# Optimization experiments

Measured on AMD Instinct MI355X. Metric: run time of the kernel, lower is better.

## Reference

```python
import jax, jax.numpy as jnp
import numpy as np
import math

N_NODES = 100000
N_EDGES = 1600000
IN_DIM = 32
OUT_DIM = 32

def setup_inputs() -> dict:
    key = jax.random.key(0)
    k1, k2, k3, k4 = jax.random.split(key, 4)
    X = jax.random.normal(k1, (N_NODES, IN_DIM), dtype=jnp.float32)
    src_idx = jax.random.randint(k2, (N_EDGES,), 0, N_NODES, dtype=jnp.int64)
    dst_idx = jax.random.randint(k3, (N_EDGES,), 0, N_NODES, dtype=jnp.int64)
    # weights init: uniform(-stdv, stdv), stdv = 1/sqrt(output_dim)
    stdv = 1.0 / math.sqrt(OUT_DIM)
    W = jax.random.uniform(k4, (IN_DIM, OUT_DIM), dtype=jnp.float32,
                           minval=-stdv, maxval=stdv)
    return {"X": X, "W": W, "src_idx": src_idx, "dst_idx": dst_idx}

def reference(X, W, src_idx, dst_idx):
    # GIN sum-aggregation SpMM: agg[i] = sum_{j in N(i)} X[j]
    agg = jax.ops.segment_sum(X[src_idx], dst_idx, num_segments=N_NODES)
    # dense GEMM: X_prime = agg @ W
    return agg @ W
```

## Files before the change

kernel.cpp:

```cpp
#include <hip/hip_runtime.h>

#define N_DIM 32
#define NPB 64
#define NB_FINE_MAX 2048
#define NC_MAX 128
#define CSH 10
#define CAPC 18432
#define CAPFINE 1280
#define CEPB 4096
#define FT 512
#define GROWS 512
#define CAPF 2048
#define MAXCH 10

__device__ __forceinline__ unsigned f2bf_rne(float f) {
    unsigned u = __float_as_uint(f);
    return (u + 0x7FFFu + ((u >> 16) & 1u)) >> 16;
}
__device__ __forceinline__ float bf2f(unsigned h) {
    return __uint_as_float(h << 16);
}

__global__ __launch_bounds__(FT) void k_fused(const float* __restrict__ X,
                                              const float* __restrict__ W,
                                              unsigned* __restrict__ Y,
                                              const int* __restrict__ src,
                                              const int* __restrict__ dst,
                                              int* __restrict__ cursorC0,
                                              int* __restrict__ tmp,
                                              int n_nodes, int n_edges,
                                              int ncoarse, int nblk_g) {
    __shared__ float Wlds[N_DIM * N_DIM];
    __shared__ int h[NC_MAX];
    __shared__ int gb[NC_MAX];
    const int t = threadIdx.x;

    if (blockIdx.x < nblk_g) {
        for (int i = t; i < N_DIM * N_DIM; i += FT) Wlds[i] = W[i];
        __syncthreads();
        const int r = blockIdx.x * GROWS + t;
        if (r >= n_nodes) return;

        float x[N_DIM];
        const float4* xr = (const float4*)(X + (size_t)r * N_DIM);
#pragma unroll
        for (int i = 0; i < N_DIM / 4; ++i) {
            float4 v = xr[i];
            x[4 * i + 0] = v.x; x[4 * i + 1] = v.y;
            x[4 * i + 2] = v.z; x[4 * i + 3] = v.w;
        }
        float acc[N_DIM];
#pragma unroll
        for (int c = 0; c < N_DIM; ++c) acc[c] = 0.0f;
#pragma unroll
        for (int k = 0; k < N_DIM; ++k) {
            const float xk = x[k];
#pragma unroll
            for (int c = 0; c < N_DIM; ++c)
                acc[c] = fmaf(xk, Wlds[k * N_DIM + c], acc[c]);
        }
        unsigned yp[16];
#pragma unroll
        for (int q = 0; q < 16; ++q)
            yp[q] = f2bf_rne(acc[2 * q]) | (f2bf_rne(acc[2 * q + 1]) << 16);
        uint4* yr = (uint4*)(Y + (size_t)r * 16);
#pragma unroll
        for (int i = 0; i < 4; ++i)
            yr[i] = make_uint4(yp[4 * i], yp[4 * i + 1],
                               yp[4 * i + 2], yp[4 * i + 3]);
    } else {
        if (t < NC_MAX) h[t] = 0;
        __syncthreads();
        const int start = (blockIdx.x - nblk_g) * CEPB;

        int vw[CEPB / FT], cw[CEPB / FT], rw[CEPB / FT];
#pragma unroll
        for (int k = 0; k < CEPB / FT; ++k) {
            int e = start + t + k * FT;
            if (e < n_edges) {
                int d = dst[e];
                int c = d >> CSH;
                cw[k] = c;
                vw[k] = src[e] | ((d & 1023) << 17);
                rw[k] = atomicAdd(&h[c], 1);
            } else {
                cw[k] = -1;
            }
        }
        __syncthreads();
        if (t < ncoarse) {
            int c = h[t];
            gb[t] = c ? atomicAdd(&cursorC0[t], c) : 0;
        }
        __syncthreads();
#pragma unroll
        for (int k = 0; k < CEPB / FT; ++k)
            if (cw[k] >= 0) {
                int idx = gb[cw[k]] + rw[k];
                if (idx < CAPC) tmp[cw[k] * CAPC + idx] = vw[k];
            }
    }
}

__global__ __launch_bounds__(256) void k_fpart(const int* __restrict__ tmp,
                                               const int* __restrict__ cursorC0,
                                               int* __restrict__ cursorF0,
                                               int* __restrict__ pairs,
                                               int ncoarse) {
    __shared__ int cnt[16], gpos[16];
    const int t = threadIdx.x;
    const int c = blockIdx.x;
    const int lenC = min(cursorC0[c], CAPC);

    for (int chunk = blockIdx.y; chunk * CAPF < lenC; chunk += gridDim.y) {
        const int start = chunk * CAPF;
        const int n = min(CAPF, lenC - start);
        if (t < 16) cnt[t] = 0;
        __syncthreads();
        int pv[CAPF / 256], rv[CAPF / 256];
#pragma unroll
        for (int k = 0; k < CAPF / 256; ++k) {
            int i = t + k * 256;
            if (i < n) {
                int p = tmp[c * CAPC + start + i];
                pv[k] = p;
                rv[k] = atomicAdd(&cnt[(p >> 23) & 15], 1);
            } else {
                pv[k] = -1;
            }
        }
        __syncthreads();
        if (t < 16) gpos[t] = cnt[t] ? atomicAdd(&cursorF0[16 * c + t], cnt[t]) : 0;
        __syncthreads();
#pragma unroll
        for (int k = 0; k < CAPF / 256; ++k) {
            if (pv[k] >= 0) {
                int p = pv[k];
                int f = (p >> 23) & 15;
                int idx = gpos[f] + rv[k];
                if (idx < CAPFINE)
                    pairs[(size_t)(16 * c + f) * CAPFINE + idx] = p & 0x7FFFFF;
            }
        }
        __syncthreads();
    }
}

__device__ __forceinline__ void addv(float* acc, uint4 v) {
    acc[0] += bf2f(v.x & 0xFFFFu); acc[1] += bf2f(v.x >> 16);
    acc[2] += bf2f(v.y & 0xFFFFu); acc[3] += bf2f(v.y >> 16);
    acc[4] += bf2f(v.z & 0xFFFFu); acc[5] += bf2f(v.z >> 16);
    acc[6] += bf2f(v.w & 0xFFFFu); acc[7] += bf2f(v.w >> 16);
}

__global__ __launch_bounds__(256) void k_agg(const uint4* __restrict__ Y4,
                                             const int* __restrict__ cursorF0,
                                             const int* __restrict__ pairs,
                                             float* __restrict__ out,
                                             int n_nodes) {
    __shared__ int sbin[CAPFINE];
    __shared__ int cnt[NPB];
    __shared__ int cst[NPB];
    __shared__ int excl[NPB];

    const int t = threadIdx.x;
    const int b = blockIdx.x;
    const int len = min(cursorF0[b], CAPFINE);
    const size_t segbase = (size_t)b * CAPFINE;
    const int g = t >> 2;
    const int l = t & 3;

    if (t < NPB) cnt[t] = 0;
    __syncthreads();

    int pv[CAPFINE / 256], rv[CAPFINE / 256];
#pragma unroll
    for (int k = 0; k < CAPFINE / 256; ++k) {
        int i = t + k * 256;
        if (i < len) {
            int p = pairs[segbase + i];
            pv[k] = p;
            rv[k] = atomicAdd(&cnt[p >> 17], 1);
        } else {
            pv[k] = -1;
        }
    }
    __syncthreads();
    if (t < 64) {
        int c0 = cnt[t];
        int c = c0;
#pragma unroll
        for (int off = 1; off < 64; off <<= 1) {
            int u = __shfl_up(c, off, 64);
            if (t >= off) c += u;
        }
        cst[t] = c;
        excl[t] = c - c0;
    }
    __syncthreads();
#pragma unroll
    for (int k = 0; k < CAPFINE / 256; ++k) {
        if (pv[k] >= 0) {
            int p = pv[k];
            sbin[excl[p >> 17] + rv[k]] = p & 0x1FFFF;
        }
    }
    __syncthreads();

    float acc[8];
#pragma unroll
    for (int i = 0; i < 8; ++i) acc[i] = 0.0f;

    const int s1 = cst[g];
    const int s0 = s1 - cnt[g];
    for (int e = s0; e < s1; e += 4) {
        const int m = s1 - e;
        int i0 = sbin[e];
        int i1 = sbin[e + ((m > 1) ? 1 : 0)];
        int i2 = sbin[e + ((m > 2) ? 2 : 0)];
        int i3 = sbin[e + ((m > 3) ? 3 : 0)];
        uint4 v0 = Y4[(size_t)i0 * 4 + l];
        uint4 v1 = Y4[(size_t)i1 * 4 + l];
        uint4 v2 = Y4[(size_t)i2 * 4 + l];
        uint4 v3 = Y4[(size_t)i3 * 4 + l];
        addv(acc, v0);
        if (m > 1) addv(acc, v1);
        if (m > 2) addv(acc, v2);
        if (m > 3) addv(acc, v3);
    }

    const int node = b * NPB + g;
    if (node < n_nodes) {
        ((float4*)out)[(size_t)node * 8 + 2 * l] =
            make_float4(acc[0], acc[1], acc[2], acc[3]);
        ((float4*)out)[(size_t)node * 8 + 2 * l + 1] =
            make_float4(acc[4], acc[5], acc[6], acc[7]);
    }
}

extern "C" void kernel_launch(void* const* d_in, const int* in_sizes, int n_in,
                              void* d_out, int out_size, void* d_ws, size_t ws_size,
                              hipStream_t stream) {
    const float* X   = (const float*)d_in[0];
    const float* W   = (const float*)d_in[1];
    const int*   src = (const int*)d_in[2];
    const int*   dst = (const int*)d_in[3];
    float* out = (float*)d_out;

    const int n_nodes = in_sizes[0] / N_DIM;
    const int n_edges = in_sizes[2];
    const int nb = (n_nodes + NPB - 1) / NPB;
    const int ncoarse = (n_nodes + 1023) / 1024;

    unsigned* Y   = (unsigned*)d_ws;
    int* cursorC0 = (int*)(Y + (size_t)n_nodes * 16);
    int* cursorF0 = cursorC0 + NC_MAX;
    int* tmp      = cursorF0 + NB_FINE_MAX;
    int* pairs    = tmp + (size_t)ncoarse * CAPC;

    const int nblk_g = (n_nodes + GROWS - 1) / GROWS;
    const int nblk_c = (n_edges + CEPB - 1) / CEPB;

    hipMemsetAsync(cursorC0, 0, (size_t)(NC_MAX + NB_FINE_MAX) * sizeof(int), stream);

    k_fused<<<nblk_g + nblk_c, FT, 0, stream>>>(X, W, Y, src, dst, cursorC0, tmp,
                                                n_nodes, n_edges, ncoarse, nblk_g);
    k_fpart<<<dim3(ncoarse, MAXCH), 256, 0, stream>>>(tmp, cursorC0, cursorF0,
                                                      pairs, ncoarse);
    k_agg<<<nb, 256, 0, stream>>>((const uint4*)Y, cursorF0, pairs, out, n_nodes);
}
```

Baseline: 127.3 us.

## Balance aggregation work by splitting sorted edges evenly across thread groups

The aggregation kernel no longer gives each 4-thread group one destination node. It now splits the block's sorted edge list into equal contiguous chunks per group. Each group accumulates runs of the same node in registers and flushes partial sums into a padded shared-memory accumulator with atomic adds, and the block then writes that accumulator to global memory. This targets load imbalance from uneven node degrees, at the cost of shared-memory atomics, extra LDS use and one more barrier.

```diff
diff --git a/kernel.cpp b/kernel.cpp
--- a/kernel.cpp
+++ b/kernel.cpp
@@ -12,6 +12,7 @@
 #define GROWS 512
 #define CAPF 2048
 #define MAXCH 10
+#define ACCW 36
 
 __device__ __forceinline__ unsigned f2bf_rne(float f) {
     unsigned u = __float_as_uint(f);
@@ -153,6 +154,16 @@
     acc[6] += bf2f(v.w & 0xFFFFu); acc[7] += bf2f(v.w >> 16);
 }
 
+__device__ __forceinline__ void flush8(float* __restrict__ accS, int node, int l,
+                                       float* __restrict__ a) {
+    float* ap = accS + node * ACCW + l * 8;
+#pragma unroll
+    for (int j = 0; j < 8; ++j) {
+        atomicAdd(ap + j, a[j]);
+        a[j] = 0.0f;
+    }
+}
+
 __global__ __launch_bounds__(256) void k_agg(const uint4* __restrict__ Y4,
                                              const int* __restrict__ cursorF0,
                                              const int* __restrict__ pairs,
@@ -160,17 +171,17 @@
                                              int n_nodes) {
     __shared__ int sbin[CAPFINE];
     __shared__ int cnt[NPB];
-    __shared__ int cst[NPB];
     __shared__ int excl[NPB];
+    __shared__ float accS[NPB * ACCW];
 
     const int t = threadIdx.x;
     const int b = blockIdx.x;
     const int len = min(cursorF0[b], CAPFINE);
     const size_t segbase = (size_t)b * CAPFINE;
-    const int g = t >> 2;
     const int l = t & 3;
 
     if (t < NPB) cnt[t] = 0;
+    for (int i = t; i < NPB * ACCW; i += 256) accS[i] = 0.0f;
     __syncthreads();
 
     int pv[CAPFINE / 256], rv[CAPFINE / 256];
@@ -194,7 +205,6 @@
             int u = __shfl_up(c, off, 64);
             if (t >= off) c += u;
         }
-        cst[t] = c;
         excl[t] = c - c0;
     }
     __syncthreads();
@@ -202,39 +212,65 @@
     for (int k = 0; k < CAPFINE / 256; ++k) {
         if (pv[k] >= 0) {
             int p = pv[k];
-            sbin[excl[p >> 17] + rv[k]] = p & 0x1FFFF;
-        }
-    }
-    __syncthreads();
-
-    float acc[8];
-#pragma unroll
-    for (int i = 0; i < 8; ++i) acc[i] = 0.0f;
-
-    const int s1 = cst[g];
-    const int s0 = s1 - cnt[g];
-    for (int e = s0; e < s1; e += 4) {
-        const int m = s1 - e;
-        int i0 = sbin[e];
-        int i1 = sbin[e + ((m > 1) ? 1 : 0)];
-        int i2 = sbin[e + ((m > 2) ? 2 : 0)];
-        int i3 = sbin[e + ((m > 3) ? 3 : 0)];
-        uint4 v0 = Y4[(size_t)i0 * 4 + l];
-        uint4 v1 = Y4[(size_t)i1 * 4 + l];
-        uint4 v2 = Y4[(size_t)i2 * 4 + l];
-        uint4 v3 = Y4[(size_t)i3 * 4 + l];
-        addv(acc, v0);
-        if (m > 1) addv(acc, v1);
-        if (m > 2) addv(acc, v2);
-        if (m > 3) addv(acc, v3);
-    }
-
-    const int node = b * NPB + g;
-    if (node < n_nodes) {
-        ((float4*)out)[(size_t)node * 8 + 2 * l] =
-            make_float4(acc[0], acc[1], acc[2], acc[3]);
-        ((float4*)out)[(size_t)node * 8 + 2 * l + 1] =
-            make_float4(acc[4], acc[5], acc[6], acc[7]);
+            sbin[excl[p >> 17] + rv[k]] = p;
+        }
+    }
+    __syncthreads();
+
+    const int s = t >> 2;
+    const int clen = (len + NPB - 1) >> 6;
+    const int e0 = s * clen;
+    const int e1 = min(e0 + clen, len);
+
+    float a[8];
+#pragma unroll
+    for (int i = 0; i < 8; ++i) a[i] = 0.0f;
+    int cur = -1;
+
+    for (int e = e0; e < e1; e += 4) {
+        const int m = e1 - e;
+        int p0 = sbin[e];
+        int p1 = sbin[e + ((m > 1) ? 1 : 0)];
+        int p2 = sbin[e + ((m > 2) ? 2 : 0)];
+        int p3 = sbin[e + ((m > 3) ? 3 : 0)];
+        uint4 v0 = Y4[(size_t)(p0 & 0x1FFFF) * 4 + l];
+        uint4 v1 = Y4[(size_t)(p1 & 0x1FFFF) * 4 + l];
+        uint4 v2 = Y4[(size_t)(p2 & 0x1FFFF) * 4 + l];
+        uint4 v3 = Y4[(size_t)(p3 & 0x1FFFF) * 4 + l];
+        int n0 = p0 >> 17;
+        if (n0 != cur) {
+            if (cur >= 0) flush8(accS, cur, l, a);
+            cur = n0;
+        }
+        addv(a, v0);
+        if (m > 1) {
+            int n1 = p1 >> 17;
+            if (n1 != cur) { flush8(accS, cur, l, a); cur = n1; }
+            addv(a, v1);
+        }
+        if (m > 2) {
+            int n2 = p2 >> 17;
+            if (n2 != cur) { flush8(accS, cur, l, a); cur = n2; }
+            addv(a, v2);
+        }
+        if (m > 3) {
+            int n3 = p3 >> 17;
+            if (n3 != cur) { flush8(accS, cur, l, a); cur = n3; }
+            addv(a, v3);
+        }
+    }
+    if (cur >= 0) flush8(accS, cur, l, a);
+    __syncthreads();
+
+    const int base = b * NPB;
+    for (int q = t; q < NPB * 8; q += 256) {
+        const int node = q >> 3;
+        const int k4 = q & 7;
+        const int gnode = base + node;
+        if (gnode < n_nodes) {
+            float4 v = *(const float4*)&accS[node * ACCW + k4 * 4];
+            ((float4*)out)[(size_t)gnode * 8 + k4] = v;
+        }
     }
 }
 
```

New measurement: 147.0 us. 15.5% more time.

## Fuse fine partitioning into aggregation kernel via per-block coarse-bucket filtering

Applied to the files above, without the earlier changes.

Removes the separate fine-partition kernel and its intermediate pairs buffer. Each aggregation block now scans its whole coarse bucket with vectorized loads and uses wave ballots to compact the entries belonging to its fine bin into shared memory. This saves a kernel launch, a global write/read round trip and part of a memset. In exchange, each coarse bucket is read redundantly by 16 blocks.

```diff
diff --git a/kernel.cpp b/kernel.cpp
--- a/kernel.cpp
+++ b/kernel.cpp
@@ -2,7 +2,6 @@
 
 #define N_DIM 32
 #define NPB 64
-#define NB_FINE_MAX 2048
 #define NC_MAX 128
 #define CSH 10
 #define CAPC 18432
@@ -10,8 +9,6 @@
 #define CEPB 4096
 #define FT 512
 #define GROWS 512
-#define CAPF 2048
-#define MAXCH 10
 
 __device__ __forceinline__ unsigned f2bf_rne(float f) {
     unsigned u = __float_as_uint(f);
@@ -102,50 +99,6 @@
     }
 }
 
-__global__ __launch_bounds__(256) void k_fpart(const int* __restrict__ tmp,
-                                               const int* __restrict__ cursorC0,
-                                               int* __restrict__ cursorF0,
-                                               int* __restrict__ pairs,
-                                               int ncoarse) {
-    __shared__ int cnt[16], gpos[16];
-    const int t = threadIdx.x;
-    const int c = blockIdx.x;
-    const int lenC = min(cursorC0[c], CAPC);
-
-    for (int chunk = blockIdx.y; chunk * CAPF < lenC; chunk += gridDim.y) {
-        const int start = chunk * CAPF;
-        const int n = min(CAPF, lenC - start);
-        if (t < 16) cnt[t] = 0;
-        __syncthreads();
-        int pv[CAPF / 256], rv[CAPF / 256];
-#pragma unroll
-        for (int k = 0; k < CAPF / 256; ++k) {
-            int i = t + k * 256;
-            if (i < n) {
-                int p = tmp[c * CAPC + start + i];
-                pv[k] = p;
-                rv[k] = atomicAdd(&cnt[(p >> 23) & 15], 1);
-            } else {
-                pv[k] = -1;
-            }
-        }
-        __syncthreads();
-        if (t < 16) gpos[t] = cnt[t] ? atomicAdd(&cursorF0[16 * c + t], cnt[t]) : 0;
-        __syncthreads();
-#pragma unroll
-        for (int k = 0; k < CAPF / 256; ++k) {
-            if (pv[k] >= 0) {
-                int p = pv[k];
-                int f = (p >> 23) & 15;
-                int idx = gpos[f] + rv[k];
-                if (idx < CAPFINE)
-                    pairs[(size_t)(16 * c + f) * CAPFINE + idx] = p & 0x7FFFFF;
-            }
-        }
-        __syncthreads();
-    }
-}
-
 __device__ __forceinline__ void addv(float* acc, uint4 v) {
     acc[0] += bf2f(v.x & 0xFFFFu); acc[1] += bf2f(v.x >> 16);
     acc[2] += bf2f(v.y & 0xFFFFu); acc[3] += bf2f(v.y >> 16);
@@ -154,33 +107,63 @@
 }
 
 __global__ __launch_bounds__(256) void k_agg(const uint4* __restrict__ Y4,
-                                             const int* __restrict__ cursorF0,
-                                             const int* __restrict__ pairs,
+                                             const int* __restrict__ cursorC0,
+                                             const int* __restrict__ tmp,
                                              float* __restrict__ out,
                                              int n_nodes) {
+    __shared__ int qbuf[CAPFINE];
     __shared__ int sbin[CAPFINE];
     __shared__ int cnt[NPB];
     __shared__ int cst[NPB];
     __shared__ int excl[NPB];
+    __shared__ int qcnt;
 
     const int t = threadIdx.x;
     const int b = blockIdx.x;
-    const int len = min(cursorF0[b], CAPFINE);
-    const size_t segbase = (size_t)b * CAPFINE;
-    const int g = t >> 2;
-    const int l = t & 3;
+    const int c = b >> 4;
+    const int f = b & 15;
+    const int lane = t & 63;
+    const int lenC = min(cursorC0[c], CAPC);
 
     if (t < NPB) cnt[t] = 0;
-    __syncthreads();
+    if (t == 0) qcnt = 0;
+    __syncthreads();
+
+    const int4* seg = (const int4*)(tmp + (size_t)c * CAPC);
+    const int nIt = (lenC + 1023) >> 10;
+    for (int k = 0; k < nIt; ++k) {
+        const int i4 = t + (k << 8);
+        const int i0 = i4 << 2;
+        int4 v = make_int4(0, 0, 0, 0);
+        if (i0 < lenC) v = seg[i4];
+        int ps[4] = {v.x, v.y, v.z, v.w};
+#pragma unroll
+        for (int j = 0; j < 4; ++j) {
+            const int p = ps[j];
+            const bool m = (i0 + j < lenC) && (((p >> 23) & 15) == f);
+            unsigned long long msk = __ballot(m);
+            if (m) {
+                int pos = __popcll(msk & ((1ull << lane) - 1ull));
+                int leader = __ffsll((unsigned long long)msk) - 1;
+                int base;
+                if (lane == leader) base = atomicAdd(&qcnt, __popcll(msk));
+                base = __shfl(base, leader, 64);
+                int idx = base + pos;
+                if (idx < CAPFINE) qbuf[idx] = p;
+            }
+        }
+    }
+    __syncthreads();
+    const int len = min(qcnt, CAPFINE);
 
     int pv[CAPFINE / 256], rv[CAPFINE / 256];
 #pragma unroll
     for (int k = 0; k < CAPFINE / 256; ++k) {
         int i = t + k * 256;
         if (i < len) {
-            int p = pairs[segbase + i];
+            int p = qbuf[i];
             pv[k] = p;
-            rv[k] = atomicAdd(&cnt[p >> 17], 1);
+            rv[k] = atomicAdd(&cnt[(p >> 17) & 63], 1);
         } else {
             pv[k] = -1;
         }
@@ -188,25 +171,27 @@
     __syncthreads();
     if (t < 64) {
         int c0 = cnt[t];
-        int c = c0;
+        int cc = c0;
 #pragma unroll
         for (int off = 1; off < 64; off <<= 1) {
-            int u = __shfl_up(c, off, 64);
-            if (t >= off) c += u;
-        }
-        cst[t] = c;
-        excl[t] = c - c0;
+            int u = __shfl_up(cc, off, 64);
+            if (t >= off) cc += u;
+        }
+        cst[t] = cc;
+        excl[t] = cc - c0;
     }
     __syncthreads();
 #pragma unroll
     for (int k = 0; k < CAPFINE / 256; ++k) {
         if (pv[k] >= 0) {
             int p = pv[k];
-            sbin[excl[p >> 17] + rv[k]] = p & 0x1FFFF;
-        }
-    }
-    __syncthreads();
-
+            sbin[excl[(p >> 17) & 63] + rv[k]] = p & 0x1FFFF;
+        }
+    }
+    __syncthreads();
+
+    const int g = t >> 2;
+    const int l = t & 3;
     float acc[8];
 #pragma unroll
     for (int i = 0; i < 8; ++i) acc[i] = 0.0f;
@@ -254,18 +239,14 @@
 
     unsigned* Y   = (unsigned*)d_ws;
     int* cursorC0 = (int*)(Y + (size_t)n_nodes * 16);
-    int* cursorF0 = cursorC0 + NC_MAX;
-    int* tmp      = cursorF0 + NB_FINE_MAX;
-    int* pairs    = tmp + (size_t)ncoarse * CAPC;
+    int* tmp      = cursorC0 + NC_MAX;
 
     const int nblk_g = (n_nodes + GROWS - 1) / GROWS;
     const int nblk_c = (n_edges + CEPB - 1) / CEPB;
 
-    hipMemsetAsync(cursorC0, 0, (size_t)(NC_MAX + NB_FINE_MAX) * sizeof(int), stream);
+    hipMemsetAsync(cursorC0, 0, (size_t)NC_MAX * sizeof(int), stream);
 
     k_fused<<<nblk_g + nblk_c, FT, 0, stream>>>(X, W, Y, src, dst, cursorC0, tmp,
                                                 n_nodes, n_edges, ncoarse, nblk_g);
-    k_fpart<<<dim3(ncoarse, MAXCH), 256, 0, stream>>>(tmp, cursorC0, cursorF0,
-                                                      pairs, ncoarse);
-    k_agg<<<nb, 256, 0, stream>>>((const uint4*)Y, cursorF0, pairs, out, n_nodes);
-}
+    k_agg<<<nb, 256, 0, stream>>>((const uint4*)Y, cursorC0, tmp, out, n_nodes);
+}
```

New measurement: 135.0 us. +6.0%, slower.

## Bucket edges directly into fine 64-node bins, removing the coarse partition pass

Applied to the files above, without the earlier changes.

Replaces the two-level partition (coarse 1024-node buckets followed by a refining k_fpart kernel) with a single pass that scatters edges straight into 1563 fine buckets of 64 nodes each. This removes one kernel launch and a full write-then-read round trip of the edge list through the tmp buffer. In exchange, each scatter block now clears and scans a 2048-entry LDS histogram, issues many more global atomics (one per nonempty fine bucket per block), and writes with less locality, scattered across many more bins.

```diff
diff --git a/kernel.cpp b/kernel.cpp
--- a/kernel.cpp
+++ b/kernel.cpp
@@ -3,15 +3,10 @@
 #define N_DIM 32
 #define NPB 64
 #define NB_FINE_MAX 2048
-#define NC_MAX 128
-#define CSH 10
-#define CAPC 18432
 #define CAPFINE 1280
 #define CEPB 4096
 #define FT 512
 #define GROWS 512
-#define CAPF 2048
-#define MAXCH 10
 
 __device__ __forceinline__ unsigned f2bf_rne(float f) {
     unsigned u = __float_as_uint(f);
@@ -26,13 +21,13 @@
                                               unsigned* __restrict__ Y,
                                               const int* __restrict__ src,
                                               const int* __restrict__ dst,
-                                              int* __restrict__ cursorC0,
-                                              int* __restrict__ tmp,
+                                              int* __restrict__ cursorF0,
+                                              int* __restrict__ pairs,
                                               int n_nodes, int n_edges,
-                                              int ncoarse, int nblk_g) {
+                                              int nb_fine, int nblk_g) {
     __shared__ float Wlds[N_DIM * N_DIM];
-    __shared__ int h[NC_MAX];
-    __shared__ int gb[NC_MAX];
+    __shared__ int h[NB_FINE_MAX];
+    __shared__ int gb[NB_FINE_MAX];
     const int t = threadIdx.x;
 
     if (blockIdx.x < nblk_g) {
@@ -69,7 +64,7 @@
             yr[i] = make_uint4(yp[4 * i], yp[4 * i + 1],
                                yp[4 * i + 2], yp[4 * i + 3]);
     } else {
-        if (t < NC_MAX) h[t] = 0;
+        for (int i = t; i < nb_fine; i += FT) h[i] = 0;
         __syncthreads();
         const int start = (blockIdx.x - nblk_g) * CEPB;
 
@@ -79,70 +74,27 @@
             int e = start + t + k * FT;
             if (e < n_edges) {
                 int d = dst[e];
-                int c = d >> CSH;
+                int c = d >> 6;
                 cw[k] = c;
-                vw[k] = src[e] | ((d & 1023) << 17);
+                vw[k] = src[e] | ((d & 63) << 17);
                 rw[k] = atomicAdd(&h[c], 1);
             } else {
                 cw[k] = -1;
             }
         }
         __syncthreads();
-        if (t < ncoarse) {
-            int c = h[t];
-            gb[t] = c ? atomicAdd(&cursorC0[t], c) : 0;
+        for (int i = t; i < nb_fine; i += FT) {
+            int c = h[i];
+            gb[i] = c ? atomicAdd(&cursorF0[i], c) : 0;
         }
         __syncthreads();
 #pragma unroll
         for (int k = 0; k < CEPB / FT; ++k)
             if (cw[k] >= 0) {
                 int idx = gb[cw[k]] + rw[k];
-                if (idx < CAPC) tmp[cw[k] * CAPC + idx] = vw[k];
+                if (idx < CAPFINE)
+                    pairs[(size_t)cw[k] * CAPFINE + idx] = vw[k];
             }
-    }
-}
-
-__global__ __launch_bounds__(256) void k_fpart(const int* __restrict__ tmp,
-                                               const int* __restrict__ cursorC0,
-                                               int* __restrict__ cursorF0,
-                                               int* __restrict__ pairs,
-                                               int ncoarse) {
-    __shared__ int cnt[16], gpos[16];
-    const int t = threadIdx.x;
-    const int c = blockIdx.x;
-    const int lenC = min(cursorC0[c], CAPC);
-
-    for (int chunk = blockIdx.y; chunk * CAPF < lenC; chunk += gridDim.y) {
-        const int start = chunk * CAPF;
-        const int n = min(CAPF, lenC - start);
-        if (t < 16) cnt[t] = 0;
-        __syncthreads();
-        int pv[CAPF / 256], rv[CAPF / 256];
-#pragma unroll
-        for (int k = 0; k < CAPF / 256; ++k) {
-            int i = t + k * 256;
-            if (i < n) {
-                int p = tmp[c * CAPC + start + i];
-                pv[k] = p;
-                rv[k] = atomicAdd(&cnt[(p >> 23) & 15], 1);
-            } else {
-                pv[k] = -1;
-            }
-        }
-        __syncthreads();
-        if (t < 16) gpos[t] = cnt[t] ? atomicAdd(&cursorF0[16 * c + t], cnt[t]) : 0;
-        __syncthreads();
-#pragma unroll
-        for (int k = 0; k < CAPF / 256; ++k) {
-            if (pv[k] >= 0) {
-                int p = pv[k];
-                int f = (p >> 23) & 15;
-                int idx = gpos[f] + rv[k];
-                if (idx < CAPFINE)
-                    pairs[(size_t)(16 * c + f) * CAPFINE + idx] = p & 0x7FFFFF;
-            }
-        }
-        __syncthreads();
     }
 }
 
@@ -250,22 +202,17 @@
     const int n_nodes = in_sizes[0] / N_DIM;
     const int n_edges = in_sizes[2];
     const int nb = (n_nodes + NPB - 1) / NPB;
-    const int ncoarse = (n_nodes + 1023) / 1024;
 
     unsigned* Y   = (unsigned*)d_ws;
-    int* cursorC0 = (int*)(Y + (size_t)n_nodes * 16);
-    int* cursorF0 = cursorC0 + NC_MAX;
-    int* tmp      = cursorF0 + NB_FINE_MAX;
-    int* pairs    = tmp + (size_t)ncoarse * CAPC;
+    int* cursorF0 = (int*)(Y + (size_t)n_nodes * 16);
+    int* pairs    = cursorF0 + NB_FINE_MAX;
 
     const int nblk_g = (n_nodes + GROWS - 1) / GROWS;
     const int nblk_c = (n_edges + CEPB - 1) / CEPB;
 
-    hipMemsetAsync(cursorC0, 0, (size_t)(NC_MAX + NB_FINE_MAX) * sizeof(int), stream);
-
-    k_fused<<<nblk_g + nblk_c, FT, 0, stream>>>(X, W, Y, src, dst, cursorC0, tmp,
-                                                n_nodes, n_edges, ncoarse, nblk_g);
-    k_fpart<<<dim3(ncoarse, MAXCH), 256, 0, stream>>>(tmp, cursorC0, cursorF0,
-                                                      pairs, ncoarse);
+    hipMemsetAsync(cursorF0, 0, (size_t)NB_FINE_MAX * sizeof(int), stream);
+
+    k_fused<<<nblk_g + nblk_c, FT, 0, stream>>>(X, W, Y, src, dst, cursorF0, pairs,
+                                                n_nodes, n_edges, nb, nblk_g);
     k_agg<<<nb, 256, 0, stream>>>((const uint4*)Y, cursorF0, pairs, out, n_nodes);
 }
```

Result: faster. 123.2 us (-3.3%).
